# Performance work log

Hardware: AMD Instinct MI355X
Metric: run time of the kernel (lower is better)

## Reference

```python
import jax, jax.numpy as jnp
import numpy as np

BN_EPS = 1e-5

def _sign(x):
    # torch-style binarize with sign(0) -> +1 (deterministic)
    return jnp.where(x >= 0, 1.0, -1.0).astype(x.dtype)

def _binarize(x):
    # straight-through estimator: forward = sign(x), backward = identity
    return x + jax.lax.stop_gradient(_sign(x) - x)

def setup_inputs() -> dict:
    key = jax.random.key(0)
    k1, k2, k3, k4 = jax.random.split(key, 4)
    B, Cin, H, Wd = 64, 512, 32, 32  # Cin = in_planes*2
    Cout = 256                        # planes == in_planes
    x = jax.random.normal(k1, (B, Cin, H, Wd), jnp.float32)
    W = jax.random.normal(k2, (Cout, Cin, 3, 3), jnp.float32) * 0.05
    gamma = 1.0 + 0.1 * jax.random.normal(k3, (Cout,), jnp.float32)
    beta = 0.1 * jax.random.normal(k4, (Cout,), jnp.float32)
    return {"x": x, "W": W, "gamma": gamma, "beta": beta}

def reference(x, W, gamma, beta):
    inplanes = x.shape[1] // 2
    residual = x[:, :inplanes]  # first half of channels, pre-binarization
    xb = _binarize(x)
    wb = _binarize(W)
    out = jax.lax.conv_general_dilated(
        xb, wb, window_strides=(1, 1), padding=((1, 1), (1, 1)),
        dimension_numbers=("NCHW", "OIHW", "NCHW"))
    # BatchNorm2d in training mode (batch statistics over N,H,W per channel)
    mean = out.mean(axis=(0, 2, 3), keepdims=True)
    var = out.var(axis=(0, 2, 3), keepdims=True)
    out = (out - mean) * jax.lax.rsqrt(var + BN_EPS)
    out = out * gamma[None, :, None, None] + beta[None, :, None, None]
    out = out + residual
    return jnp.clip(out, -1.0, 1.0)  # Hardtanh
```

## Files before the change

### kernel.cpp

```cpp
#include <hip/hip_runtime.h>

#define CIN   512
#define COUT  256
#define HWDIM 32
#define NBATCH 64
#define PIX_PER_IMG (HWDIM * HWDIM)
#define NPIX (NBATCH * PIX_PER_IMG)

typedef __attribute__((ext_vector_type(4))) int   i32x4;
typedef __attribute__((ext_vector_type(8))) int   i32x8;
typedef __attribute__((ext_vector_type(4))) float f32x4;

#define OFF_XB4   ((size_t)0)
#define OFF_WB4   ((size_t)16777216)
#define OFF_CONV  ((size_t)17367040)
#define OFF_PSUM  ((size_t)50921472)
#define OFF_PSQ   ((size_t)51445760)
#define OFF_SCALE ((size_t)52494336)
#define OFF_SHIFT (OFF_SCALE + 1024)
#define OFF_ZERO  (OFF_SHIFT + 1024)

#define NIB(v) ((v) >= 0.f ? 0x2u : 0xAu)

__global__ __launch_bounds__(256) void pack_x4_kernel(const float* __restrict__ x,
                                                      unsigned char* __restrict__ xb4) {
  const int plane = blockIdx.x;
  const int n = plane >> 5, h = plane & 31;
  __shared__ unsigned int tile[HWDIM * 66];
  const int t = threadIdx.x;
  const float* xp = x + (size_t)n * CIN * PIX_PER_IMG + (size_t)h * HWDIM;
#pragma unroll
  for (int it = 0; it < 2; ++it) {
    int idx = it * 256 + t;
    int cib = idx >> 3;
    int w4 = (idx & 7) << 2;
    unsigned n0 = 0, n1 = 0, n2 = 0, n3 = 0;
#pragma unroll
    for (int d = 0; d < 8; ++d) {
      float4 f = *reinterpret_cast<const float4*>(
          xp + (size_t)(cib * 8 + d) * PIX_PER_IMG + w4);
      n0 |= NIB(f.x) << (4 * d);
      n1 |= NIB(f.y) << (4 * d);
      n2 |= NIB(f.z) << (4 * d);
      n3 |= NIB(f.w) << (4 * d);
    }
    tile[(w4 + 0) * 66 + cib] = n0;
    tile[(w4 + 1) * 66 + cib] = n1;
    tile[(w4 + 2) * 66 + cib] = n2;
    tile[(w4 + 3) * 66 + cib] = n3;
  }
  __syncthreads();
  uint4* xo = reinterpret_cast<uint4*>(xb4 + (size_t)plane * (HWDIM * CIN / 2));
#pragma unroll
  for (int it = 0; it < 2; ++it) {
    int cc = it * 256 + t;
    int w = cc >> 4, c4 = (cc & 15) << 2;
    uint4 v = make_uint4(tile[w * 66 + c4], tile[w * 66 + c4 + 1],
                         tile[w * 66 + c4 + 2], tile[w * 66 + c4 + 3]);
    xo[cc] = v;
  }
}

__global__ __launch_bounds__(256) void pack_w4_kernel(const float* __restrict__ W,
                                                      unsigned int* __restrict__ wb4,
                                                      unsigned int* __restrict__ zpw) {
  if (blockIdx.x == 576) {
    zpw[threadIdx.x] = 0u;
    return;
  }
  int idxu = blockIdx.x * 256 + threadIdx.x;
  int tap = idxu / (COUT * 64);
  int rem = idxu - tap * (COUT * 64);
  int co = rem >> 6;
  int ci0 = (rem & 63) << 3;
  unsigned nib = 0;
#pragma unroll
  for (int d = 0; d < 8; ++d) {
    float v = W[((size_t)co * CIN + ci0 + d) * 9 + tap];
    nib |= NIB(v) << (4 * d);
  }
  wb4[idxu] = nib;
}

#define BM 256
#define BKB 64
#define ABYTES (BM * BKB)
#define BUFB   (ABYTES + COUT * BKB)
#define LDS_TOTAL (4 * BUFB)
#define TAPB4 (COUT * (CIN / 2))

__device__ __forceinline__ void load16(const void* g, void* l) {
  __builtin_amdgcn_global_load_lds((const __attribute__((address_space(1))) void*)g,
                                   (__attribute__((address_space(3))) void*)l, 16, 0, 0);
}

__device__ __forceinline__ i32x8 up8(i32x4 v) {
  i32x8 r;
  r[0] = v[0]; r[1] = v[1]; r[2] = v[2]; r[3] = v[3];
  r[4] = 0;    r[5] = 0;    r[6] = 0;    r[7] = 0;
  return r;
}

__global__ __launch_bounds__(512, 2) void conv_kernel(
    const unsigned char* __restrict__ xb4,
    const unsigned char* __restrict__ wb4,
    short* __restrict__ cv,
    const unsigned char* __restrict__ zp,
    int* __restrict__ psum,
    long long* __restrict__ psq) {
  extern __shared__ signed char lds[];
  const int t = threadIdx.x;
  const int wid = t >> 6, lane = t & 63;
  const int b = blockIdx.x;
  const int nimg = b >> 2;
  const int h0 = (b & 3) * 8;

  const int wr = wid >> 2;
  const int wc = wid & 3;

  f32x4 acc[8][4];
#pragma unroll
  for (int m = 0; m < 8; ++m)
#pragma unroll
    for (int n = 0; n < 4; ++n) { f32x4 z = {0.f, 0.f, 0.f, 0.f}; acc[m][n] = z; }

  auto abase = [&](int tap, int c) -> const unsigned char* {
    int r = c >> 2;
    int sw = ((c & 3) ^ ((c >> 3) & 3)) << 4;
    int dh = tap / 3 - 1, dw = tap % 3 - 1;
    int hs = h0 + (r >> 5) + dh;
    int ws2 = (r & 31) + dw;
    bool ok = ((unsigned)hs < 32u) && ((unsigned)ws2 < 32u);
    return ok ? xb4 + (size_t)((nimg * 32 + hs) * 32 + ws2) * 256 + sw
              : zp + sw;
  };
  auto bbase = [&](int tap, int c) -> const unsigned char* {
    int co = c >> 2;
    int sw = ((c & 3) ^ ((c >> 3) & 3)) << 4;
    return wb4 + (size_t)tap * TAPB4 + (size_t)co * 256 + sw;
  };

  const int c0 = t, c1 = 512 + t;
  const unsigned char *a0 = abase(0, c0), *a1 = abase(0, c1);
  const unsigned char *b0 = bbase(0, c0), *b1 = bbase(0, c1);

  const int koff = (lane >> 4) << 4;
  const int ksw  = (((lane >> 1) & 3) << 4);
  int aoff[8], boff[4];
#pragma unroll
  for (int m = 0; m < 8; ++m) {
    int row = wr * 128 + m * 16 + (lane & 15);
    aoff[m] = row * BKB + (koff ^ ksw);
  }
#pragma unroll
  for (int n = 0; n < 4; ++n) {
    int col = wc * 64 + n * 16 + (lane & 15);
    boff[n] = ABYTES + col * BKB + (koff ^ ksw);
  }

  auto stage = [&](int buf, const unsigned char* A0, const unsigned char* A1,
                   const unsigned char* B0, const unsigned char* B1, int off) {
    signed char* dst = lds + buf * BUFB;
    load16(A0 + off, (void*)(dst + c0 * 16));
    load16(A1 + off, (void*)(dst + c1 * 16));
    load16(B0 + off, (void*)(dst + ABYTES + c0 * 16));
    load16(B1 + off, (void*)(dst + ABYTES + c1 * 16));
  };

  auto compute = [&](int buf) {
    const signed char* base = lds + buf * BUFB;
    i32x4 af[8], bf[4];
#pragma unroll
    for (int n = 0; n < 4; ++n)
      bf[n] = *reinterpret_cast<const i32x4*>(base + boff[n]);
#pragma unroll
    for (int m = 0; m < 8; ++m)
      af[m] = *reinterpret_cast<const i32x4*>(base + aoff[m]);
    __builtin_amdgcn_s_setprio(1);
#pragma unroll
    for (int m = 0; m < 8; ++m)
#pragma unroll
      for (int n = 0; n < 4; ++n)
        acc[m][n] = __builtin_amdgcn_mfma_scale_f32_16x16x128_f8f6f4(
            up8(af[m]), up8(bf[n]), acc[m][n],
            4, 4,
            0, 0x7F7F7F7Fu,
            0, 0x7F7F7F7Fu);
    __builtin_amdgcn_s_setprio(0);
  };

  stage(0, a0, a1, b0, b1, 0);
  stage(1, a0, a1, b0, b1, 64);
  asm volatile("s_waitcnt vmcnt(0)" ::: "memory");
  __builtin_amdgcn_s_barrier();

  for (int tap = 0; tap < 9; ++tap) {
    const unsigned char *na0, *na1, *nb0, *nb1;
    if (tap < 8) {
      na0 = abase(tap + 1, c0); na1 = abase(tap + 1, c1);
      nb0 = b0 + TAPB4;         nb1 = b1 + TAPB4;
    } else {
      na0 = na1 = nb0 = nb1 = zp;
    }
    stage(2, a0, a1, b0, b1, 128);
    stage(3, a0, a1, b0, b1, 192);
    compute(0);
    compute(1);
    asm volatile("s_waitcnt vmcnt(0)" ::: "memory");
    __builtin_amdgcn_s_barrier();
    if (tap < 8) {
      stage(0, na0, na1, nb0, nb1, 0);
      stage(1, na0, na1, nb0, nb1, 64);
    }
    compute(2);
    compute(3);
    asm volatile("s_waitcnt vmcnt(0)" ::: "memory");
    __builtin_amdgcn_s_barrier();

    a0 = na0; a1 = na1; b0 = nb0; b1 = nb1;
  }

  const int P0 = b * BM;
#pragma unroll
  for (int m = 0; m < 8; ++m) {
#pragma unroll
    for (int n = 0; n < 4; ++n) {
      int row = wr * 128 + m * 16 + ((lane >> 4) << 2);
      int co = wc * 64 + n * 16 + (lane & 15);
      int P = P0 + row;
      int ni = P >> 10;
      int hw = P & 1023;
      short4 v = make_short4((short)(int)acc[m][n][0], (short)(int)acc[m][n][1],
                             (short)(int)acc[m][n][2], (short)(int)acc[m][n][3]);
      *reinterpret_cast<short4*>(cv + (((size_t)ni * COUT + co) << 10) + hw) = v;
    }
  }

  const int slot = b * 2 + wr;
#pragma unroll
  for (int n = 0; n < 4; ++n) {
    int s1 = 0;
    long long s2 = 0;
#pragma unroll
    for (int m = 0; m < 8; ++m)
#pragma unroll
      for (int j = 0; j < 4; ++j) {
        int v = (int)acc[m][n][j];
        s1 += v;
        s2 += (long long)v * v;
      }
    s1 += __shfl_xor(s1, 16, 64);
    s1 += __shfl_xor(s1, 32, 64);
    s2 += __shfl_xor(s2, 16, 64);
    s2 += __shfl_xor(s2, 32, 64);
    if (lane < 16) {
      int c = wc * 64 + n * 16 + lane;
      psum[(size_t)c * 512 + slot] = s1;
      psq[(size_t)c * 512 + slot] = s2;
    }
  }
}

__global__ __launch_bounds__(64) void stats_kernel(const int* __restrict__ psum,
                                                   const long long* __restrict__ psq,
                                                   const float* __restrict__ gamma,
                                                   const float* __restrict__ beta,
                                                   float* __restrict__ scale,
                                                   float* __restrict__ shift) {
  const int co = blockIdx.x;
  const int l = threadIdx.x;
  const int* ps = psum + (size_t)co * 512;
  const long long* pq = psq + (size_t)co * 512;
  long long s1 = 0, s2 = 0;
#pragma unroll
  for (int i = 0; i < 8; ++i) {
    s1 += ps[l * 8 + i];
    s2 += pq[l * 8 + i];
  }
#pragma unroll
  for (int off = 32; off > 0; off >>= 1) {
    s1 += __shfl_xor(s1, off, 64);
    s2 += __shfl_xor(s2, off, 64);
  }
  if (l == 0) {
    double cnt = (double)NPIX;
    double mean = (double)s1 / cnt;
    double ex2 = (double)s2 / cnt;
    double var = ex2 - mean * mean;
    double rs = 1.0 / sqrt(var + 1e-5);
    float g = gamma[co];
    scale[co] = (float)rs * g;
    shift[co] = beta[co] - (float)(mean * rs) * g;
  }
}

__global__ __launch_bounds__(256) void final_kernel(const short* __restrict__ cv,
                                                    const float* __restrict__ x,
                                                    const float* __restrict__ scale,
                                                    const float* __restrict__ shift,
                                                    float* __restrict__ out) {
  size_t i = ((size_t)blockIdx.x * 256 + threadIdx.x) * 8;
  int co = (int)((i >> 10) & 255);
  size_t n = i >> 18;
  size_t hw = i & 1023;
  short4 c0 = *reinterpret_cast<const short4*>(cv + i);
  short4 c1 = *reinterpret_cast<const short4*>(cv + i + 4);
  const float* xr = x + ((n * CIN + co) << 10) + hw;
  float4 r0 = *reinterpret_cast<const float4*>(xr);
  float4 r1 = *reinterpret_cast<const float4*>(xr + 4);
  float sc = scale[co], sh = shift[co];
  float4 o0, o1;
  o0.x = fminf(1.f, fmaxf(-1.f, (float)c0.x * sc + sh + r0.x));
  o0.y = fminf(1.f, fmaxf(-1.f, (float)c0.y * sc + sh + r0.y));
  o0.z = fminf(1.f, fmaxf(-1.f, (float)c0.z * sc + sh + r0.z));
  o0.w = fminf(1.f, fmaxf(-1.f, (float)c0.w * sc + sh + r0.w));
  o1.x = fminf(1.f, fmaxf(-1.f, (float)c1.x * sc + sh + r1.x));
  o1.y = fminf(1.f, fmaxf(-1.f, (float)c1.y * sc + sh + r1.y));
  o1.z = fminf(1.f, fmaxf(-1.f, (float)c1.z * sc + sh + r1.z));
  o1.w = fminf(1.f, fmaxf(-1.f, (float)c1.w * sc + sh + r1.w));
  *reinterpret_cast<float4*>(out + i) = o0;
  *reinterpret_cast<float4*>(out + i + 4) = o1;
}

extern "C" void kernel_launch(void* const* d_in, const int* in_sizes, int n_in,
                              void* d_out, int out_size, void* d_ws, size_t ws_size,
                              hipStream_t stream) {
  const float* x     = (const float*)d_in[0];
  const float* W     = (const float*)d_in[1];
  const float* gamma = (const float*)d_in[2];
  const float* beta  = (const float*)d_in[3];
  float* out = (float*)d_out;
  char* ws = (char*)d_ws;

  unsigned char* xb4 = (unsigned char*)(ws + OFF_XB4);
  unsigned char* wb4 = (unsigned char*)(ws + OFF_WB4);
  short* cv = (short*)(ws + OFF_CONV);
  int* psum = (int*)(ws + OFF_PSUM);
  long long* psq = (long long*)(ws + OFF_PSQ);
  float* scale = (float*)(ws + OFF_SCALE);
  float* shift = (float*)(ws + OFF_SHIFT);
  unsigned char* zp = (unsigned char*)(ws + OFF_ZERO);

  hipFuncSetAttribute((const void*)conv_kernel,
                      hipFuncAttributeMaxDynamicSharedMemorySize, LDS_TOTAL);

  pack_x4_kernel<<<NBATCH * HWDIM, 256, 0, stream>>>(x, xb4);
  pack_w4_kernel<<<577, 256, 0, stream>>>(W, (unsigned int*)wb4, (unsigned int*)zp);
  conv_kernel<<<NPIX / BM, 512, LDS_TOTAL, stream>>>(xb4, wb4, cv, zp, psum, psq);
  stats_kernel<<<COUT, 64, 0, stream>>>(psum, psq, gamma, beta, scale, shift);
  final_kernel<<<(NBATCH * COUT * PIX_PER_IMG) / (256 * 8), 256, 0, stream>>>(
      cv, x, scale, shift, out);
}
```

Measured before the change: 104.4 us.

## Halve conv M-tile to 128 and switch to double-buffered per-K-step pipeline

```diff
diff --git a/kernel.cpp b/kernel.cpp
--- a/kernel.cpp
+++ b/kernel.cpp
@@ -15,8 +15,8 @@
 #define OFF_WB4   ((size_t)16777216)
 #define OFF_CONV  ((size_t)17367040)
 #define OFF_PSUM  ((size_t)50921472)
-#define OFF_PSQ   ((size_t)51445760)
-#define OFF_SCALE ((size_t)52494336)
+#define OFF_PSQ   ((size_t)51970048)
+#define OFF_SCALE ((size_t)54067200)
 #define OFF_SHIFT (OFF_SCALE + 1024)
 #define OFF_ZERO  (OFF_SHIFT + 1024)
 
@@ -82,11 +82,10 @@
   wb4[idxu] = nib;
 }
 
-#define BM 256
+#define BM 128
 #define BKB 64
 #define ABYTES (BM * BKB)
 #define BUFB   (ABYTES + COUT * BKB)
-#define LDS_TOTAL (4 * BUFB)
 #define TAPB4 (COUT * (CIN / 2))
 
 __device__ __forceinline__ void load16(const void* g, void* l) {
@@ -101,32 +100,32 @@
   return r;
 }
 
-__global__ __launch_bounds__(512, 2) void conv_kernel(
+__global__ __launch_bounds__(512, 4) void conv_kernel(
     const unsigned char* __restrict__ xb4,
     const unsigned char* __restrict__ wb4,
     short* __restrict__ cv,
     const unsigned char* __restrict__ zp,
     int* __restrict__ psum,
     long long* __restrict__ psq) {
-  extern __shared__ signed char lds[];
+  __shared__ signed char lds[2][BUFB];
   const int t = threadIdx.x;
   const int wid = t >> 6, lane = t & 63;
   const int b = blockIdx.x;
-  const int nimg = b >> 2;
-  const int h0 = (b & 3) * 8;
+  const int nimg = b >> 3;
+  const int h0 = (b & 7) * 4;
 
   const int wr = wid >> 2;
   const int wc = wid & 3;
 
-  f32x4 acc[8][4];
-#pragma unroll
-  for (int m = 0; m < 8; ++m)
+  f32x4 acc[4][4];
+#pragma unroll
+  for (int m = 0; m < 4; ++m)
 #pragma unroll
     for (int n = 0; n < 4; ++n) { f32x4 z = {0.f, 0.f, 0.f, 0.f}; acc[m][n] = z; }
 
-  auto abase = [&](int tap, int c) -> const unsigned char* {
-    int r = c >> 2;
-    int sw = ((c & 3) ^ ((c >> 3) & 3)) << 4;
+  auto abase = [&](int tap) -> const unsigned char* {
+    int r = t >> 2;
+    int sw = ((t & 3) ^ ((t >> 3) & 3)) << 4;
     int dh = tap / 3 - 1, dw = tap % 3 - 1;
     int hs = h0 + (r >> 5) + dh;
     int ws2 = (r & 31) + dw;
@@ -134,22 +133,22 @@
     return ok ? xb4 + (size_t)((nimg * 32 + hs) * 32 + ws2) * 256 + sw
               : zp + sw;
   };
-  auto bbase = [&](int tap, int c) -> const unsigned char* {
+  auto bbase = [&](int c) -> const unsigned char* {
     int co = c >> 2;
     int sw = ((c & 3) ^ ((c >> 3) & 3)) << 4;
-    return wb4 + (size_t)tap * TAPB4 + (size_t)co * 256 + sw;
+    return wb4 + (size_t)co * 256 + sw;
   };
 
-  const int c0 = t, c1 = 512 + t;
-  const unsigned char *a0 = abase(0, c0), *a1 = abase(0, c1);
-  const unsigned char *b0 = bbase(0, c0), *b1 = bbase(0, c1);
+  const unsigned char* a0 = abase(0);
+  const unsigned char* b0 = bbase(t);
+  const unsigned char* b1 = bbase(512 + t);
 
   const int koff = (lane >> 4) << 4;
   const int ksw  = (((lane >> 1) & 3) << 4);
-  int aoff[8], boff[4];
-#pragma unroll
-  for (int m = 0; m < 8; ++m) {
-    int row = wr * 128 + m * 16 + (lane & 15);
+  int aoff[4], boff[4];
+#pragma unroll
+  for (int m = 0; m < 4; ++m) {
+    int row = wr * 64 + m * 16 + (lane & 15);
     aoff[m] = row * BKB + (koff ^ ksw);
   }
 #pragma unroll
@@ -158,27 +157,26 @@
     boff[n] = ABYTES + col * BKB + (koff ^ ksw);
   }
 
-  auto stage = [&](int buf, const unsigned char* A0, const unsigned char* A1,
-                   const unsigned char* B0, const unsigned char* B1, int off) {
-    signed char* dst = lds + buf * BUFB;
-    load16(A0 + off, (void*)(dst + c0 * 16));
-    load16(A1 + off, (void*)(dst + c1 * 16));
-    load16(B0 + off, (void*)(dst + ABYTES + c0 * 16));
-    load16(B1 + off, (void*)(dst + ABYTES + c1 * 16));
+  auto stage = [&](int buf, const unsigned char* A0, const unsigned char* B0,
+                   const unsigned char* B1, int off) {
+    signed char* dst = &lds[buf][0];
+    load16(A0 + off, (void*)(dst + t * 16));
+    load16(B0 + off, (void*)(dst + ABYTES + t * 16));
+    load16(B1 + off, (void*)(dst + ABYTES + (512 + t) * 16));
   };
 
   auto compute = [&](int buf) {
-    const signed char* base = lds + buf * BUFB;
-    i32x4 af[8], bf[4];
+    const signed char* base = &lds[buf][0];
+    i32x4 af[4], bf[4];
 #pragma unroll
     for (int n = 0; n < 4; ++n)
       bf[n] = *reinterpret_cast<const i32x4*>(base + boff[n]);
 #pragma unroll
-    for (int m = 0; m < 8; ++m)
+    for (int m = 0; m < 4; ++m)
       af[m] = *reinterpret_cast<const i32x4*>(base + aoff[m]);
     __builtin_amdgcn_s_setprio(1);
 #pragma unroll
-    for (int m = 0; m < 8; ++m)
+    for (int m = 0; m < 4; ++m)
 #pragma unroll
       for (int n = 0; n < 4; ++n)
         acc[m][n] = __builtin_amdgcn_mfma_scale_f32_16x16x128_f8f6f4(
@@ -189,43 +187,34 @@
     __builtin_amdgcn_s_setprio(0);
   };
 
-  stage(0, a0, a1, b0, b1, 0);
-  stage(1, a0, a1, b0, b1, 64);
+  stage(0, a0, b0, b1, 0);
   asm volatile("s_waitcnt vmcnt(0)" ::: "memory");
   __builtin_amdgcn_s_barrier();
 
   for (int tap = 0; tap < 9; ++tap) {
-    const unsigned char *na0, *na1, *nb0, *nb1;
-    if (tap < 8) {
-      na0 = abase(tap + 1, c0); na1 = abase(tap + 1, c1);
-      nb0 = b0 + TAPB4;         nb1 = b1 + TAPB4;
-    } else {
-      na0 = na1 = nb0 = nb1 = zp;
+#pragma unroll
+    for (int j = 0; j < 4; ++j) {
+      const int s = tap * 4 + j;
+      if (j < 3) {
+        stage((s + 1) & 1, a0, b0, b1, (j + 1) * 64);
+      } else if (tap < 8) {
+        const unsigned char* an = abase(tap + 1);
+        stage((s + 1) & 1, an, b0 + TAPB4, b1 + TAPB4, 0);
+        a0 = an;
+      }
+      compute(s & 1);
+      asm volatile("s_waitcnt vmcnt(0)" ::: "memory");
+      __builtin_amdgcn_s_barrier();
     }
-    stage(2, a0, a1, b0, b1, 128);
-    stage(3, a0, a1, b0, b1, 192);
-    compute(0);
-    compute(1);
-    asm volatile("s_waitcnt vmcnt(0)" ::: "memory");
-    __builtin_amdgcn_s_barrier();
-    if (tap < 8) {
-      stage(0, na0, na1, nb0, nb1, 0);
-      stage(1, na0, na1, nb0, nb1, 64);
-    }
-    compute(2);
-    compute(3);
-    asm volatile("s_waitcnt vmcnt(0)" ::: "memory");
-    __builtin_amdgcn_s_barrier();
-
-    a0 = na0; a1 = na1; b0 = nb0; b1 = nb1;
+    b0 += TAPB4; b1 += TAPB4;
   }
 
   const int P0 = b * BM;
 #pragma unroll
-  for (int m = 0; m < 8; ++m) {
+  for (int m = 0; m < 4; ++m) {
 #pragma unroll
     for (int n = 0; n < 4; ++n) {
-      int row = wr * 128 + m * 16 + ((lane >> 4) << 2);
+      int row = wr * 64 + m * 16 + ((lane >> 4) << 2);
       int co = wc * 64 + n * 16 + (lane & 15);
       int P = P0 + row;
       int ni = P >> 10;
@@ -242,7 +231,7 @@
     int s1 = 0;
     long long s2 = 0;
 #pragma unroll
-    for (int m = 0; m < 8; ++m)
+    for (int m = 0; m < 4; ++m)
 #pragma unroll
       for (int j = 0; j < 4; ++j) {
         int v = (int)acc[m][n][j];
@@ -255,8 +244,8 @@
     s2 += __shfl_xor(s2, 32, 64);
     if (lane < 16) {
       int c = wc * 64 + n * 16 + lane;
-      psum[(size_t)c * 512 + slot] = s1;
-      psq[(size_t)c * 512 + slot] = s2;
+      psum[(size_t)c * 1024 + slot] = s1;
+      psq[(size_t)c * 1024 + slot] = s2;
     }
   }
 }
@@ -269,13 +258,13 @@
                                                    float* __restrict__ shift) {
   const int co = blockIdx.x;
   const int l = threadIdx.x;
-  const int* ps = psum + (size_t)co * 512;
-  const long long* pq = psq + (size_t)co * 512;
+  const int* ps = psum + (size_t)co * 1024;
+  const long long* pq = psq + (size_t)co * 1024;
   long long s1 = 0, s2 = 0;
 #pragma unroll
-  for (int i = 0; i < 8; ++i) {
-    s1 += ps[l * 8 + i];
-    s2 += pq[l * 8 + i];
+  for (int i = 0; i < 16; ++i) {
+    s1 += ps[l * 16 + i];
+    s2 += pq[l * 16 + i];
   }
 #pragma unroll
   for (int off = 32; off > 0; off >>= 1) {
@@ -341,12 +330,9 @@
   float* shift = (float*)(ws + OFF_SHIFT);
   unsigned char* zp = (unsigned char*)(ws + OFF_ZERO);
 
-  hipFuncSetAttribute((const void*)conv_kernel,
-                      hipFuncAttributeMaxDynamicSharedMemorySize, LDS_TOTAL);
-
   pack_x4_kernel<<<NBATCH * HWDIM, 256, 0, stream>>>(x, xb4);
   pack_w4_kernel<<<577, 256, 0, stream>>>(W, (unsigned int*)wb4, (unsigned int*)zp);
-  conv_kernel<<<NPIX / BM, 512, LDS_TOTAL, stream>>>(xb4, wb4, cv, zp, psum, psq);
+  conv_kernel<<<NPIX / BM, 512, 0, stream>>>(xb4, wb4, cv, zp, psum, psq);
   stats_kernel<<<COUT, 64, 0, stream>>>(psum, psq, gamma, beta, scale, shift);
   final_kernel<<<(NBATCH * COUT * PIX_PER_IMG) / (256 * 8), 256, 0, stream>>>(
       cv, x, scale, shift, out);
```

New measurement: 101.9 us, median of 2. 1.02x faster.
